# Kernel tuning notes

Measured on AMD Instinct MI355X. Metric: run time of the kernel, lower is better.

Reference implementation:

```python
import jax, jax.numpy as jnp
import numpy as np

DIM = 128
IN_DIM = 2
LAYERS = 4
H = 256
W = 256
WH = W // 2 + 1  # rfft last-dim size
RATIO = 1.0


def _radial_mask():
    # waves = sqrt(k^2 + r^2) over the rfft2 grid; keep waves <= (W//2)*ratio
    k = np.fft.rfftfreq(W) * W            # (WH,)
    r = np.fft.fftfreq(H) * H             # (H,)
    waves = np.sqrt(k[None, :] ** 2 + r[:, None] ** 2)  # (H, WH)
    return jnp.asarray(waves <= (W // 2) * RATIO)


def conv1x1(x, w, b):
    # x: (b,c,h,w), w: (o,c), b: (o,)
    return jnp.einsum('bchw,oc->bohw', x, w) + b[None, :, None, None]


def setup_inputs() -> dict:
    key = jax.random.key(0)
    ks = jax.random.split(key, 15)
    d = DIM
    inp = {
        'x': jax.random.normal(ks[0], (4, IN_DIM, H, W), dtype=jnp.float32),
        'enc_w': jax.random.normal(ks[1], (d, IN_DIM), dtype=jnp.float32) * (1.0 / np.sqrt(IN_DIM)),
        'enc_b': jnp.zeros((d,), dtype=jnp.float32),
        'pos_emb': jax.random.normal(ks[2], (1, d, H, W), dtype=jnp.float32) * 0.02,
        'mlp_w1': jax.random.normal(ks[3], (LAYERS, 4 * d, d), dtype=jnp.float32) * (1.0 / np.sqrt(d)),
        'mlp_b1': jnp.zeros((LAYERS, 4 * d), dtype=jnp.float32),
        'mlp_w2': jax.random.normal(ks[4], (LAYERS, d, 4 * d), dtype=jnp.float32) * (1.0 / np.sqrt(4 * d)),
        'mlp_b2': jnp.zeros((LAYERS, d), dtype=jnp.float32),
        'spec_mags': jax.random.normal(ks[5], (LAYERS, d, H, WH), dtype=jnp.float32),
        'spec_phases': jax.random.normal(ks[6], (LAYERS, d, H, WH), dtype=jnp.float32),
        'oxo_w': jax.random.normal(ks[7], (LAYERS, d, d), dtype=jnp.float32) * (1.0 / np.sqrt(d)),
        'oxo_b': jnp.zeros((LAYERS, d), dtype=jnp.float32),
        'dec_w': jax.random.normal(ks[8], (IN_DIM, d), dtype=jnp.float32) * (1.0 / np.sqrt(d)),
        'dec_b': jnp.zeros((IN_DIM,), dtype=jnp.float32),
    }
    return inp


def reference(x, enc_w, enc_b, pos_emb, mlp_w1, mlp_b1, mlp_w2, mlp_b2,
              spec_mags, spec_phases, oxo_w, oxo_b, dec_w, dec_b):
    scale = (DIM / IN_DIM) ** 0.5
    mask = _radial_mask()  # (H, WH) bool, constant
    h = conv1x1(x, enc_w, enc_b) * scale + pos_emb
    for i in range(LAYERS):
        # mlp block: 1x1 conv -> SiLU -> 1x1 conv
        x1 = jax.nn.silu(conv1x1(h, mlp_w1[i], mlp_b1[i]))
        x1 = conv1x1(x1, mlp_w2[i], mlp_b2[i])
        # spectral conv: rfft2 (ortho), complex filter on radially-masked modes,
        # zeros elsewhere (equivalent to masked_select/scatter in the original), irfft2
        xf = jnp.fft.rfft2(x1, norm='ortho')  # (b,c,H,WH) complex64
        filt = jax.nn.sigmoid(spec_mags[i]) * jnp.exp(1j * spec_phases[i])  # (c,H,WH)
        xf = jnp.where(mask[None, None, :, :], xf * filt[None], 0.0 + 0.0j)
        x1 = jnp.fft.irfft2(xf, s=(H, W), norm='ortho')
        x1 = conv1x1(x1, oxo_w[i], oxo_b[i])
        h = x1 + h
    return conv1x1(h, dec_w, dec_b) / scale
```

## Files before the change

kernel.cpp:

```cpp
#include <hip/hip_runtime.h>
#include <math.h>

#define PI2 6.2831853071795864769f

typedef short bf16x8 __attribute__((ext_vector_type(8)));
typedef float f32x4 __attribute__((ext_vector_type(4)));
typedef int   i32x4 __attribute__((ext_vector_type(4)));

__device__ inline unsigned splitf(float v) {
    unsigned u  = __float_as_uint(v);
    unsigned r  = (u + 0x7fffu + ((u >> 16) & 1u)) >> 16;
    float hi    = __uint_as_float(r << 16);
    float lof   = v - hi;
    unsigned u2 = __float_as_uint(lof);
    unsigned r2 = (u2 + 0x7fffu + ((u2 >> 16) & 1u)) >> 16;
    return (r & 0xffffu) | (r2 << 16);
}
__device__ inline float upk(unsigned w) {
    return __uint_as_float(w << 16) + __uint_as_float(w & 0xffff0000u);
}

union VecU { i32x4 i; bf16x8 s; };

__device__ inline void unpack2(i32x4 d0, i32x4 d1, bf16x8& hi, bf16x8& lo) {
    VecU h, l;
    h.i.x = __builtin_amdgcn_perm(d0.y, d0.x, 0x05040100);
    h.i.y = __builtin_amdgcn_perm(d0.w, d0.z, 0x05040100);
    h.i.z = __builtin_amdgcn_perm(d1.y, d1.x, 0x05040100);
    h.i.w = __builtin_amdgcn_perm(d1.w, d1.z, 0x05040100);
    l.i.x = __builtin_amdgcn_perm(d0.y, d0.x, 0x07060302);
    l.i.y = __builtin_amdgcn_perm(d0.w, d0.z, 0x07060302);
    l.i.z = __builtin_amdgcn_perm(d1.y, d1.x, 0x07060302);
    l.i.w = __builtin_amdgcn_perm(d1.w, d1.z, 0x07060302);
    hi = h.s; lo = l.s;
}

__device__ inline void unpack8(const int* d, bf16x8& hi, bf16x8& lo) {
    VecU h, l;
    h.i.x = __builtin_amdgcn_perm(d[1], d[0], 0x05040100);
    h.i.y = __builtin_amdgcn_perm(d[3], d[2], 0x05040100);
    h.i.z = __builtin_amdgcn_perm(d[5], d[4], 0x05040100);
    h.i.w = __builtin_amdgcn_perm(d[7], d[6], 0x05040100);
    l.i.x = __builtin_amdgcn_perm(d[1], d[0], 0x07060302);
    l.i.y = __builtin_amdgcn_perm(d[3], d[2], 0x07060302);
    l.i.z = __builtin_amdgcn_perm(d[5], d[4], 0x07060302);
    l.i.w = __builtin_amdgcn_perm(d[7], d[6], 0x07060302);
    hi = h.s; lo = l.s;
}

__global__ void sentinel_kernel(float* __restrict__ out, int n) {
    int t = blockIdx.x * 256 + threadIdx.x;
    if (t < n) out[t] = 12345.0f;
}

__global__ void split_kernel(const float* __restrict__ in, unsigned* __restrict__ out) {
    long q = (long)blockIdx.x * 256 + threadIdx.x;
    const float4* ip = (const float4*)in;
    float4 v = ip[q];
    i32x4 o;
    o.x = (int)splitf(v.x); o.y = (int)splitf(v.y);
    o.z = (int)splitf(v.z); o.w = (int)splitf(v.w);
    ((i32x4*)out)[q] = o;
}

__global__ void enc_kernel(const float* __restrict__ x, const float* __restrict__ w,
                           const float* __restrict__ b, const float* __restrict__ pos,
                           unsigned* __restrict__ h) {
    long t = (long)blockIdx.x * 256 + threadIdx.x;
    int pq = (int)(t & 16383);
    int c  = (int)((t >> 14) & 127);
    int bb = (int)(t >> 21);
    float4 x0 = *(const float4*)(x + ((long)bb * 2 + 0) * 65536 + pq * 4);
    float4 x1 = *(const float4*)(x + ((long)bb * 2 + 1) * 65536 + pq * 4);
    float4 pv = *(const float4*)(pos + (long)c * 65536 + pq * 4);
    float w0 = w[c * 2], w1 = w[c * 2 + 1], bc = b[c];
    uint4 o;
    o.x = splitf((w0 * x0.x + w1 * x1.x + bc) * 8.0f + pv.x);
    o.y = splitf((w0 * x0.y + w1 * x1.y + bc) * 8.0f + pv.y);
    o.z = splitf((w0 * x0.z + w1 * x1.z + bc) * 8.0f + pv.z);
    o.w = splitf((w0 * x0.w + w1 * x1.w + bc) * 8.0f + pv.w);
    *(uint4*)(h + t * 4) = o;
}

__global__ __launch_bounds__(256, 2)
void mlp_fused(const unsigned* __restrict__ Ax, const unsigned* __restrict__ W1x,
               const float* __restrict__ b1, const unsigned* __restrict__ W2x,
               const float* __restrict__ b2, float* __restrict__ t2) {
    __shared__ unsigned SM[12800];
    unsigned* ALDS = SM;
    unsigned* HLDS = SM + 8448;
    int tid = threadIdx.x;
    int w = tid >> 6, l = tid & 63;
    int lr = l & 15, lg = l >> 4;
    int p0 = blockIdx.x * 64;

#pragma unroll
    for (int i = 0; i < 8; i++) {
        int f = i * 256 + tid;
        int k = f >> 4, q = f & 15;
        uint4 v = *(const uint4*)(Ax + (long)k * 65536 + p0 + q * 4);
        ALDS[(q * 4 + 0) * 132 + k] = v.x;
        ALDS[(q * 4 + 1) * 132 + k] = v.y;
        ALDS[(q * 4 + 2) * 132 + k] = v.z;
        ALDS[(q * 4 + 3) * 132 + k] = v.w;
    }
    __syncthreads();

    f32x4 acc2[4][2] = {};
#pragma unroll 1
    for (int c = 0; c < 8; c++) {
        f32x4 acc1[4] = {};
#pragma unroll
        for (int ks = 0; ks < 4; ks++) {
            bf16x8 bh, bl;
            {
                const unsigned* bp = W1x + (c * 64 + w * 16 + lr) * 128 + ks * 32 + lg * 8;
                i32x4 d0 = *(const i32x4*)bp;
                i32x4 d1 = *(const i32x4*)(bp + 4);
                unpack2(d0, d1, bh, bl);
            }
#pragma unroll
            for (int ms = 0; ms < 4; ms++) {
                const i32x4* apx = (const i32x4*)&ALDS[(ms * 16 + lr) * 132 + ks * 32 + lg * 8];
                i32x4 a0 = apx[0], a1 = apx[1];
                bf16x8 ah, al; unpack2(a0, a1, ah, al);
                acc1[ms] = __builtin_amdgcn_mfma_f32_16x16x32_bf16(ah, bh, acc1[ms], 0, 0, 0);
                acc1[ms] = __builtin_amdgcn_mfma_f32_16x16x32_bf16(ah, bl, acc1[ms], 0, 0, 0);
                acc1[ms] = __builtin_amdgcn_mfma_f32_16x16x32_bf16(al, bh, acc1[ms], 0, 0, 0);
            }
        }
        {
            int hl = w * 16 + lr;
            float bias = b1[c * 64 + hl];
#pragma unroll
            for (int ms = 0; ms < 4; ms++)
#pragma unroll
                for (int r = 0; r < 4; r++) {
                    float pre = acc1[ms][r] + bias;
                    float s = pre / (1.0f + __expf(-pre));
                    int pix = ms * 16 + lg * 4 + r;
                    HLDS[pix * 68 + hl] = splitf(s);
                }
        }
        __syncthreads();
#pragma unroll
        for (int ks2 = 0; ks2 < 2; ks2++) {
            bf16x8 bh[2], bl[2];
#pragma unroll
            for (int ns = 0; ns < 2; ns++) {
                const unsigned* bp = W2x + (w * 32 + ns * 16 + lr) * 512 + c * 64 + ks2 * 32 + lg * 8;
                i32x4 d0 = *(const i32x4*)bp;
                i32x4 d1 = *(const i32x4*)(bp + 4);
                unpack2(d0, d1, bh[ns], bl[ns]);
            }
#pragma unroll
            for (int ms = 0; ms < 4; ms++) {
                const i32x4* hp = (const i32x4*)&HLDS[(ms * 16 + lr) * 68 + ks2 * 32 + lg * 8];
                i32x4 d0 = hp[0], d1 = hp[1];
                bf16x8 ah, al; unpack2(d0, d1, ah, al);
#pragma unroll
                for (int ns = 0; ns < 2; ns++) {
                    acc2[ms][ns] = __builtin_amdgcn_mfma_f32_16x16x32_bf16(ah, bh[ns], acc2[ms][ns], 0, 0, 0);
                    acc2[ms][ns] = __builtin_amdgcn_mfma_f32_16x16x32_bf16(ah, bl[ns], acc2[ms][ns], 0, 0, 0);
                    acc2[ms][ns] = __builtin_amdgcn_mfma_f32_16x16x32_bf16(al, bh[ns], acc2[ms][ns], 0, 0, 0);
                }
            }
        }
        __syncthreads();
    }
    float* T = (float*)SM;
#pragma unroll
    for (int ns = 0; ns < 2; ns++) {
        int n = w * 32 + ns * 16 + lr;
        float bias = b2[n];
#pragma unroll
        for (int ms = 0; ms < 4; ms++)
#pragma unroll
            for (int r = 0; r < 4; r++) {
                int pix = ms * 16 + lg * 4 + r;
                T[n * 68 + pix] = acc2[ms][ns][r] + bias;
            }
    }
    __syncthreads();
#pragma unroll
    for (int i = 0; i < 8; i++) {
        int f = i * 256 + tid;
        int n = f >> 4, q = f & 15;
        float4 v = *(const float4*)&T[n * 68 + q * 4];
        *(float4*)(t2 + (long)n * 65536 + p0 + q * 4) = v;
    }
}

__global__ __launch_bounds__(256, 2)
void oxo_kernel(const unsigned* __restrict__ Tx, const unsigned* __restrict__ Bx,
                const float* __restrict__ ob, unsigned* __restrict__ h) {
    __shared__ float T[128 * 128];
    int tid = threadIdx.x;
    int w = tid >> 6, l = tid & 63;
    int lr = l & 15, lg = l >> 4;
    int m0 = blockIdx.x * 128;
    int n0 = w * 32;
    f32x4 acc[8][2] = {};
    for (int k0 = 0; k0 < 128; k0 += 32) {
        bf16x8 bh[2], bl[2];
#pragma unroll
        for (int ns = 0; ns < 2; ns++) {
            const unsigned* bp = Bx + (n0 + ns * 16 + lr) * 128 + k0 + lg * 8;
            i32x4 d0 = *(const i32x4*)bp;
            i32x4 d1 = *(const i32x4*)(bp + 4);
            unpack2(d0, d1, bh[ns], bl[ns]);
        }
#pragma unroll
        for (int ms = 0; ms < 8; ms++) {
            const unsigned* ap = Tx + (long)(k0 + lg * 8) * 65536 + m0 + ms * 16 + lr;
            int d[8];
#pragma unroll
            for (int j = 0; j < 8; j++) d[j] = (int)ap[(long)j * 65536];
            bf16x8 ah, al; unpack8(d, ah, al);
#pragma unroll
            for (int ns = 0; ns < 2; ns++) {
                acc[ms][ns] = __builtin_amdgcn_mfma_f32_16x16x32_bf16(ah, bh[ns], acc[ms][ns], 0, 0, 0);
                acc[ms][ns] = __builtin_amdgcn_mfma_f32_16x16x32_bf16(ah, bl[ns], acc[ms][ns], 0, 0, 0);
                acc[ms][ns] = __builtin_amdgcn_mfma_f32_16x16x32_bf16(al, bh[ns], acc[ms][ns], 0, 0, 0);
            }
        }
    }
#pragma unroll
    for (int ns = 0; ns < 2; ns++) {
        int n = n0 + ns * 16 + lr;
#pragma unroll
        for (int ms = 0; ms < 8; ms++) {
            int blk = ((ms * 4 + lg) + n) & 31;
#pragma unroll
            for (int r = 0; r < 4; r++)
                T[n * 128 + blk * 4 + r] = acc[ms][ns][r];
        }
    }
    __syncthreads();
#pragma unroll
    for (int i = 0; i < 16; i++) {
        int flat = i * 256 + tid;
        int n = flat >> 5, q = flat & 31;
        const float4* src = (const float4*)&T[n * 128 + (((q + n) & 31) * 4)];
        float4 v = *src;
        float bias = ob[n];
        unsigned* hp = h + (long)n * 65536 + m0 + q * 4;
        uint4 hv = *(uint4*)hp;
        uint4 o;
        o.x = splitf(upk(hv.x) + v.x + bias);
        o.y = splitf(upk(hv.y) + v.y + bias);
        o.z = splitf(upk(hv.z) + v.z + bias);
        o.w = splitf(upk(hv.w) + v.w + bias);
        *(uint4*)hp = o;
    }
}

__global__ void fft_row_fwd(const float* __restrict__ in, float2* __restrict__ freq, int c0) {
    __shared__ float2 A[4][256];
    __shared__ float2 B[4][256];
    __shared__ float2 TW[128];
    int tid = threadIdx.x;
    int pr = blockIdx.x >> 6, rgrp = blockIdx.x & 63;
    if (tid < 128) {
        float sn, cs; __sincosf((PI2 / 256.f) * (float)tid, &sn, &cs);
        TW[tid] = make_float2(cs, sn);
    }
    {
        int r = tid >> 6, l = tid & 63;
        int row = rgrp * 4 + r;
        const float4* sa = (const float4*)(in + ((long)(c0 + pr * 2 + 0) * 256 + row) * 256);
        const float4* sb = (const float4*)(in + ((long)(c0 + pr * 2 + 1) * 256 + row) * 256);
        float4 va = sa[l], vb = sb[l];
        A[r][l * 4 + 0] = make_float2(va.x, vb.x);
        A[r][l * 4 + 1] = make_float2(va.y, vb.y);
        A[r][l * 4 + 2] = make_float2(va.z, vb.z);
        A[r][l * 4 + 3] = make_float2(va.w, vb.w);
    }
    __syncthreads();
    float2 (*s)[256] = A; float2 (*d)[256] = B;
    for (int m = 1; m < 256; m <<= 1) {
#pragma unroll
        for (int q = 0; q < 2; q++) {
            int bf = tid + q * 256;
            int r = bf >> 7, i = bf & 127;
            int jm = i & ~(m - 1);
            float2 c0v = s[r][i], c1 = s[r][i + 128];
            float2 t = TW[jm];
            float2 df = make_float2(c0v.x - c1.x, c0v.y - c1.y);
            d[r][i + jm]     = make_float2(c0v.x + c1.x, c0v.y + c1.y);
            d[r][i + jm + m] = make_float2(t.x * df.x + t.y * df.y, t.x * df.y - t.y * df.x);
        }
        __syncthreads();
        float2 (*tmp)[256] = s; s = d; d = tmp;
    }
    long iba = (long)(pr * 2 + 0) * 34816;
    long ibb = (long)(pr * 2 + 1) * 34816;
    for (int q = tid; q < 4 * 129; q += 256) {
        int r = q / 129; int k = q - r * 129;
        float2 z  = s[r][k];
        float2 zm = s[r][(256 - k) & 255];
        float2 za = make_float2(0.5f * (z.x + zm.x), 0.5f * (z.y - zm.y));
        float2 zb = make_float2(0.5f * (z.y + zm.y), 0.5f * (zm.x - z.x));
        long off = (k >> 3) * 2048 + (rgrp * 4 + r) * 8 + (k & 7);
        freq[iba + off] = za;
        freq[ibb + off] = zb;
    }
}

__global__ void fft_col(float2* __restrict__ freq, const float* __restrict__ mags,
                        const float* __restrict__ phases, int c0) {
    __shared__ float2 A[8][256];
    __shared__ float2 B[8][256];
    __shared__ float2 TW[128];
    int tid = threadIdx.x;
    int img = blockIdx.x / 17;
    int kt  = blockIdx.x % 17;
    int kx0 = kt * 8;
    float2* base = freq + (long)img * 34816 + kt * 2048;
    if (tid < 128) {
        float sn, cs; __sincosf((PI2 / 256.f) * (float)tid, &sn, &cs);
        TW[tid] = make_float2(cs, sn);
    }
#pragma unroll
    for (int q = 0; q < 8; q++) {
        int e = tid + q * 256;
        A[e & 7][e >> 3] = base[e];
    }
    __syncthreads();
    float2 (*s)[256] = A; float2 (*d)[256] = B;
    for (int m = 1; m < 256; m <<= 1) {
#pragma unroll
        for (int q = 0; q < 4; q++) {
            int bf = tid + q * 256;
            int cl = bf >> 7, i = bf & 127;
            int jm = i & ~(m - 1);
            float2 c0v = s[cl][i], c1 = s[cl][i + 128];
            float2 t = TW[jm];
            float2 df = make_float2(c0v.x - c1.x, c0v.y - c1.y);
            d[cl][i + jm]     = make_float2(c0v.x + c1.x, c0v.y + c1.y);
            d[cl][i + jm + m] = make_float2(t.x * df.x + t.y * df.y, t.x * df.y - t.y * df.x);
        }
        __syncthreads();
        float2 (*tmp)[256] = s; s = d; d = tmp;
    }
#pragma unroll
    for (int q = 0; q < 8; q++) {
        int e = tid + q * 256;
        int cl = e & 7, ky = e >> 3;
        int kx = kx0 + cl;
        float2 v = s[cl][ky];
        float2 r = make_float2(0.f, 0.f);
        if (kx < 129) {
            int ry = ky < 128 ? ky : ky - 256;
            if (kx * kx + ry * ry <= 16384) {
                long fi = ((long)(c0 + img) * 256 + ky) * 129 + kx;
                float mg = mags[fi], ph = phases[fi];
                float sg = 1.0f / (1.0f + __expf(-mg));
                float sn, cs; __sincosf(ph, &sn, &cs);
                float fr = sg * cs, fim = sg * sn;
                r = make_float2(v.x * fr - v.y * fim, v.x * fim + v.y * fr);
            }
        }
        s[cl][ky] = r;
    }
    __syncthreads();
    for (int m = 1; m < 256; m <<= 1) {
#pragma unroll
        for (int q = 0; q < 4; q++) {
            int bf = tid + q * 256;
            int cl = bf >> 7, i = bf & 127;
            int jm = i & ~(m - 1);
            float2 c0v = s[cl][i], c1 = s[cl][i + 128];
            float2 t = TW[jm];
            float2 df = make_float2(c0v.x - c1.x, c0v.y - c1.y);
            d[cl][i + jm]     = make_float2(c0v.x + c1.x, c0v.y + c1.y);
            d[cl][i + jm + m] = make_float2(t.x * df.x - t.y * df.y, t.x * df.y + t.y * df.x);
        }
        __syncthreads();
        float2 (*tmp)[256] = s; s = d; d = tmp;
    }
#pragma unroll
    for (int q = 0; q < 8; q++) {
        int e = tid + q * 256;
        base[e] = s[e & 7][e >> 3];
    }
}

__global__ void fft_row_inv(const float2* __restrict__ freq, unsigned* __restrict__ out, int c0) {
    __shared__ float2 A[4][256];
    __shared__ float2 B[4][256];
    __shared__ float2 TW[128];
    int tid = threadIdx.x;
    int pr = blockIdx.x >> 6, rgrp = blockIdx.x & 63;
    if (tid < 128) {
        float sn, cs; __sincosf((PI2 / 256.f) * (float)tid, &sn, &cs);
        TW[tid] = make_float2(cs, sn);
    }
    long iba = (long)(pr * 2 + 0) * 34816;
    long ibb = (long)(pr * 2 + 1) * 34816;
#pragma unroll
    for (int q = 0; q < 4; q++) {
        int e = tid + q * 256;
        int r = e >> 8, xx = e & 255;
        int k = (xx <= 128) ? xx : 256 - xx;
        long off = (k >> 3) * 2048 + (rgrp * 4 + r) * 8 + (k & 7);
        float2 ga = freq[iba + off];
        float2 gb = freq[ibb + off];
        if (k == 0 || k == 128) { ga.y = 0.f; gb.y = 0.f; }
        float2 v;
        if (xx <= 128) v = make_float2(ga.x - gb.y, ga.y + gb.x);
        else           v = make_float2(ga.x + gb.y, gb.x - ga.y);
        A[r][xx] = v;
    }
    __syncthreads();
    float2 (*s)[256] = A; float2 (*d)[256] = B;
    for (int m = 1; m < 256; m <<= 1) {
#pragma unroll
        for (int q = 0; q < 2; q++) {
            int bf = tid + q * 256;
            int r = bf >> 7, i = bf & 127;
            int jm = i & ~(m - 1);
            float2 c0v = s[r][i], c1 = s[r][i + 128];
            float2 t = TW[jm];
            float2 df = make_float2(c0v.x - c1.x, c0v.y - c1.y);
            d[r][i + jm]     = make_float2(c0v.x + c1.x, c0v.y + c1.y);
            d[r][i + jm + m] = make_float2(t.x * df.x - t.y * df.y, t.x * df.y + t.y * df.x);
        }
        __syncthreads();
        float2 (*tmp)[256] = s; s = d; d = tmp;
    }
    {
        int r = tid >> 6, l = tid & 63;
        const float sc = 1.0f / 65536.0f;
        int row = rgrp * 4 + r;
        uint4 oa, ob;
        oa.x = splitf(s[r][l * 4 + 0].x * sc);
        oa.y = splitf(s[r][l * 4 + 1].x * sc);
        oa.z = splitf(s[r][l * 4 + 2].x * sc);
        oa.w = splitf(s[r][l * 4 + 3].x * sc);
        ob.x = splitf(s[r][l * 4 + 0].y * sc);
        ob.y = splitf(s[r][l * 4 + 1].y * sc);
        ob.z = splitf(s[r][l * 4 + 2].y * sc);
        ob.w = splitf(s[r][l * 4 + 3].y * sc);
        *(uint4*)(out + ((long)(c0 + pr * 2 + 0) * 256 + row) * 256 + l * 4) = oa;
        *(uint4*)(out + ((long)(c0 + pr * 2 + 1) * 256 + row) * 256 + l * 4) = ob;
    }
}

__global__ void dec_kernel(const unsigned* __restrict__ h, const float* __restrict__ w,
                           const float* __restrict__ b, float* __restrict__ out) {
    int t = blockIdx.x * 256 + threadIdx.x;
    int bb = t >> 16, p = t & 65535;
    const unsigned* hb = h + (long)bb * 8388608 + p;
    float a0 = b[0], a1 = b[1];
    float a0b = 0.f, a1b = 0.f;
#pragma unroll 4
    for (int c = 0; c < 128; c += 2) {
        float h0 = upk(hb[(long)c * 65536]);
        float h1 = upk(hb[(long)(c + 1) * 65536]);
        a0  += w[c] * h0;        a1  += w[128 + c] * h0;
        a0b += w[c + 1] * h1;    a1b += w[128 + c + 1] * h1;
    }
    out[((long)bb * 2 + 0) * 65536 + p] = (a0 + a0b) * 0.125f;
    out[((long)bb * 2 + 1) * 65536 + p] = (a1 + a1b) * 0.125f;
}

extern "C" void kernel_launch(void* const* d_in, const int* in_sizes, int n_in,
                              void* d_out, int out_size, void* d_ws, size_t ws_size,
                              hipStream_t stream) {
    const float* x        = (const float*)d_in[0];
    const float* enc_w    = (const float*)d_in[1];
    const float* enc_b    = (const float*)d_in[2];
    const float* pos_emb  = (const float*)d_in[3];
    const float* mlp_w1   = (const float*)d_in[4];
    const float* mlp_b1   = (const float*)d_in[5];
    const float* mlp_w2   = (const float*)d_in[6];
    const float* mlp_b2   = (const float*)d_in[7];
    const float* spec_mag = (const float*)d_in[8];
    const float* spec_ph  = (const float*)d_in[9];
    const float* oxo_w    = (const float*)d_in[10];
    const float* oxo_b    = (const float*)d_in[11];
    const float* dec_w    = (const float*)d_in[12];
    const float* dec_b    = (const float*)d_in[13];
    float* outp = (float*)d_out;

    const size_t WS_NEEDED = 186187776ULL;
    if (ws_size < WS_NEEDED) {
        sentinel_kernel<<<(out_size + 255) / 256, 256, 0, stream>>>(outp, out_size);
        return;
    }

    unsigned* u    = (unsigned*)d_ws;
    unsigned* h    = u;
    float*    t2   = (float*)(u + 33554432);
    unsigned* TxO  = (unsigned*)t2;
    float2*   freq = (float2*)(u + 41943040);
    unsigned* Wx1  = u + 46399488;
    unsigned* Wx2  = Wx1 + 65536;
    unsigned* Wox  = Wx2 + 65536;

    enc_kernel<<<32768, 256, 0, stream>>>(x, enc_w, enc_b, pos_emb, h);

    for (int l = 0; l < 4; l++) {
        split_kernel<<<64, 256, 0, stream>>>(mlp_w1 + (long)l * 65536, Wx1);
        split_kernel<<<64, 256, 0, stream>>>(mlp_w2 + (long)l * 65536, Wx2);
        split_kernel<<<16, 256, 0, stream>>>(oxo_w + (long)l * 16384, Wox);
        const float* b1l = mlp_b1 + l * 512;
        const float* b2l = mlp_b2 + l * 128;
        const float* mgl = spec_mag + (long)l * 4227072;
        const float* phl = spec_ph  + (long)l * 4227072;
        const float* obl = oxo_b + l * 128;
        for (int b = 0; b < 4; b++) {
            unsigned* hb = h + (long)b * 8388608;
            mlp_fused<<<1024, 256, 0, stream>>>(hb, Wx1, b1l, Wx2, b2l, t2);
            for (int c0 = 0; c0 < 128; c0 += 64) {
                fft_row_fwd<<<2048, 256, 0, stream>>>(t2, freq, c0);
                fft_col<<<64 * 17, 256, 0, stream>>>(freq, mgl, phl, c0);
                fft_row_inv<<<2048, 256, 0, stream>>>(freq, TxO, c0);
            }
            oxo_kernel<<<512, 256, 0, stream>>>(TxO, Wox, obl, hb);
        }
    }

    dec_kernel<<<1024, 256, 0, stream>>>(h, dec_w, dec_b, outp);
}
```

Before: 3.700 ms.

## Give each wave its own pixel rows in mlp_fused and drop block barriers

The fused MLP kernel changes its work split. Each wave now owns 16 pixels across all hidden and output channels, instead of all 64 pixels for a slice of channels. The SiLU hidden tile goes to a wave-private LDS region, which removes the two __syncthreads per hidden chunk, and the output staging reuses the wave's own slice of the input tile. Launch bounds rise to 3 blocks per CU. In exchange, every wave now loads the full W1/W2 weight panels from global/L1, roughly four times more weight traffic per block, and register pressure under the tighter occupancy bound may cause spills.

```diff
diff --git a/kernel.cpp b/kernel.cpp
--- a/kernel.cpp
+++ b/kernel.cpp
@@ -82,17 +82,17 @@
     *(uint4*)(h + t * 4) = o;
 }
 
-__global__ __launch_bounds__(256, 2)
+__global__ __launch_bounds__(256, 3)
 void mlp_fused(const unsigned* __restrict__ Ax, const unsigned* __restrict__ W1x,
                const float* __restrict__ b1, const unsigned* __restrict__ W2x,
                const float* __restrict__ b2, float* __restrict__ t2) {
     __shared__ unsigned SM[12800];
     unsigned* ALDS = SM;
-    unsigned* HLDS = SM + 8448;
     int tid = threadIdx.x;
     int w = tid >> 6, l = tid & 63;
     int lr = l & 15, lg = l >> 4;
     int p0 = blockIdx.x * 64;
+    unsigned* HW = SM + 8448 + w * 1088;
 
 #pragma unroll
     for (int i = 0; i < 8; i++) {
@@ -106,88 +106,71 @@
     }
     __syncthreads();
 
-    f32x4 acc2[4][2] = {};
+    f32x4 acc2[8] = {};
 #pragma unroll 1
     for (int c = 0; c < 8; c++) {
         f32x4 acc1[4] = {};
 #pragma unroll
         for (int ks = 0; ks < 4; ks++) {
-            bf16x8 bh, bl;
-            {
-                const unsigned* bp = W1x + (c * 64 + w * 16 + lr) * 128 + ks * 32 + lg * 8;
+            const i32x4* apx = (const i32x4*)&ALDS[(w * 16 + lr) * 132 + ks * 32 + lg * 8];
+            i32x4 a0 = apx[0], a1 = apx[1];
+            bf16x8 ah, al; unpack2(a0, a1, ah, al);
+#pragma unroll
+            for (int ns = 0; ns < 4; ns++) {
+                const unsigned* bp = W1x + (c * 64 + ns * 16 + lr) * 128 + ks * 32 + lg * 8;
                 i32x4 d0 = *(const i32x4*)bp;
                 i32x4 d1 = *(const i32x4*)(bp + 4);
-                unpack2(d0, d1, bh, bl);
+                bf16x8 bh, bl; unpack2(d0, d1, bh, bl);
+                acc1[ns] = __builtin_amdgcn_mfma_f32_16x16x32_bf16(ah, bh, acc1[ns], 0, 0, 0);
+                acc1[ns] = __builtin_amdgcn_mfma_f32_16x16x32_bf16(ah, bl, acc1[ns], 0, 0, 0);
+                acc1[ns] = __builtin_amdgcn_mfma_f32_16x16x32_bf16(al, bh, acc1[ns], 0, 0, 0);
             }
-#pragma unroll
-            for (int ms = 0; ms < 4; ms++) {
-                const i32x4* apx = (const i32x4*)&ALDS[(ms * 16 + lr) * 132 + ks * 32 + lg * 8];
-                i32x4 a0 = apx[0], a1 = apx[1];
-                bf16x8 ah, al; unpack2(a0, a1, ah, al);
-                acc1[ms] = __builtin_amdgcn_mfma_f32_16x16x32_bf16(ah, bh, acc1[ms], 0, 0, 0);
-                acc1[ms] = __builtin_amdgcn_mfma_f32_16x16x32_bf16(ah, bl, acc1[ms], 0, 0, 0);
-                acc1[ms] = __builtin_amdgcn_mfma_f32_16x16x32_bf16(al, bh, acc1[ms], 0, 0, 0);
+        }
+#pragma unroll
+        for (int ns = 0; ns < 4; ns++) {
+            float bias = b1[c * 64 + ns * 16 + lr];
+#pragma unroll
+            for (int r = 0; r < 4; r++) {
+                float pre = acc1[ns][r] + bias;
+                float s = pre / (1.0f + __expf(-pre));
+                HW[(lg * 4 + r) * 68 + ns * 16 + lr] = splitf(s);
             }
         }
-        {
-            int hl = w * 16 + lr;
-            float bias = b1[c * 64 + hl];
-#pragma unroll
-            for (int ms = 0; ms < 4; ms++)
-#pragma unroll
-                for (int r = 0; r < 4; r++) {
-                    float pre = acc1[ms][r] + bias;
-                    float s = pre / (1.0f + __expf(-pre));
-                    int pix = ms * 16 + lg * 4 + r;
-                    HLDS[pix * 68 + hl] = splitf(s);
-                }
-        }
-        __syncthreads();
 #pragma unroll
         for (int ks2 = 0; ks2 < 2; ks2++) {
-            bf16x8 bh[2], bl[2];
-#pragma unroll
-            for (int ns = 0; ns < 2; ns++) {
-                const unsigned* bp = W2x + (w * 32 + ns * 16 + lr) * 512 + c * 64 + ks2 * 32 + lg * 8;
+            const i32x4* hp = (const i32x4*)&HW[lr * 68 + ks2 * 32 + lg * 8];
+            i32x4 h0 = hp[0], h1 = hp[1];
+            bf16x8 ah, al; unpack2(h0, h1, ah, al);
+#pragma unroll
+            for (int ns = 0; ns < 8; ns++) {
+                const unsigned* bp = W2x + (ns * 16 + lr) * 512 + c * 64 + ks2 * 32 + lg * 8;
                 i32x4 d0 = *(const i32x4*)bp;
                 i32x4 d1 = *(const i32x4*)(bp + 4);
-                unpack2(d0, d1, bh[ns], bl[ns]);
+                bf16x8 bh, bl; unpack2(d0, d1, bh, bl);
+                acc2[ns] = __builtin_amdgcn_mfma_f32_16x16x32_bf16(ah, bh, acc2[ns], 0, 0, 0);
+                acc2[ns] = __builtin_amdgcn_mfma_f32_16x16x32_bf16(ah, bl, acc2[ns], 0, 0, 0);
+                acc2[ns] = __builtin_amdgcn_mfma_f32_16x16x32_bf16(al, bh, acc2[ns], 0, 0, 0);
             }
-#pragma unroll
-            for (int ms = 0; ms < 4; ms++) {
-                const i32x4* hp = (const i32x4*)&HLDS[(ms * 16 + lr) * 68 + ks2 * 32 + lg * 8];
-                i32x4 d0 = hp[0], d1 = hp[1];
-                bf16x8 ah, al; unpack2(d0, d1, ah, al);
-#pragma unroll
-                for (int ns = 0; ns < 2; ns++) {
-                    acc2[ms][ns] = __builtin_amdgcn_mfma_f32_16x16x32_bf16(ah, bh[ns], acc2[ms][ns], 0, 0, 0);
-                    acc2[ms][ns] = __builtin_amdgcn_mfma_f32_16x16x32_bf16(ah, bl[ns], acc2[ms][ns], 0, 0, 0);
-                    acc2[ms][ns] = __builtin_amdgcn_mfma_f32_16x16x32_bf16(al, bh[ns], acc2[ms][ns], 0, 0, 0);
-                }
-            }
-        }
-        __syncthreads();
-    }
-    float* T = (float*)SM;
-#pragma unroll
-    for (int ns = 0; ns < 2; ns++) {
-        int n = w * 32 + ns * 16 + lr;
+        }
+    }
+    float4* T4 = (float4*)(ALDS + (long)w * 16 * 132);
+#pragma unroll
+    for (int ns = 0; ns < 8; ns++) {
+        int n = ns * 16 + lr;
         float bias = b2[n];
-#pragma unroll
-        for (int ms = 0; ms < 4; ms++)
-#pragma unroll
-            for (int r = 0; r < 4; r++) {
-                int pix = ms * 16 + lg * 4 + r;
-                T[n * 68 + pix] = acc2[ms][ns][r] + bias;
-            }
-    }
-    __syncthreads();
-#pragma unroll
-    for (int i = 0; i < 8; i++) {
-        int f = i * 256 + tid;
-        int n = f >> 4, q = f & 15;
-        float4 v = *(const float4*)&T[n * 68 + q * 4];
-        *(float4*)(t2 + (long)n * 65536 + p0 + q * 4) = v;
+        float4 v;
+        v.x = acc2[ns][0] + bias;
+        v.y = acc2[ns][1] + bias;
+        v.z = acc2[ns][2] + bias;
+        v.w = acc2[ns][3] + bias;
+        T4[n * 4 + lg] = v;
+    }
+#pragma unroll
+    for (int it = 0; it < 8; it++) {
+        int f = it * 64 + l;
+        int n = f >> 2, q = f & 3;
+        float4 v = T4[n * 4 + q];
+        *(float4*)(t2 + (long)n * 65536 + p0 + w * 16 + q * 4) = v;
     }
 }
 
```

Measured after the change: 6.438 ms. +74.0%, slower.
